# Kernel optimization log

Hardware: AMD Instinct MI355X
Metric: run time of the kernel (lower is better)

## Reference

```python
import jax, jax.numpy as jnp
import numpy as np

H = 2          # h_dim (hard-coded in PPIModel)
L = 4          # n_hid rgcn layers
R = 16         # num_rels
B = 8          # num_bases
N = 1_000_000  # num_nodes
E = 16_000_000 # num_edges


def setup_inputs() -> dict:
    key = jax.random.key(0)
    ks = jax.random.split(key, 10)
    features = jax.random.normal(ks[0], (N * H,), dtype=jnp.float32)
    edge_src = jax.random.randint(ks[1], (E,), 0, N)
    edge_dst = jax.random.randint(ks[2], (E,), 0, N)
    edge_type = jax.random.randint(ks[3], (E,), 0, R)
    norm = jax.random.uniform(ks[4], (E, 1), dtype=jnp.float32)
    # Basis-decomposition params per layer: W_r = sum_b comp[r,b] * V[b]
    V = jax.random.normal(ks[5], (L, B, H, H), dtype=jnp.float32) / np.sqrt(H)
    comp = jax.random.normal(ks[6], (L, R, B), dtype=jnp.float32) / np.sqrt(B)
    bias = jnp.zeros((L, H), dtype=jnp.float32)  # DGL RelGraphConv h_bias (default bias=True)
    w_mlp = jax.random.normal(ks[7], (1, N * H), dtype=jnp.float32) / np.sqrt(N * H)
    b_mlp = jnp.zeros((1,), dtype=jnp.float32)
    return dict(features=features, norm=norm, V=V, comp=comp, bias=bias,
                w_mlp=w_mlp, b_mlp=b_mlp,
                edge_src=edge_src, edge_dst=edge_dst, edge_type=edge_type)


def reference(features, norm, V, comp, bias, w_mlp, b_mlp, edge_src, edge_dst, edge_type):
    x = features.reshape(-1, H)          # [N, 2]
    skip = x
    for i in range(L):
        # relation weights from bases: [R, H, H]
        W = jnp.einsum('rb,bio->rio', comp[i], V[i])
        # message per edge: gather src feats, apply relation weight, scale by norm
        msg = jnp.einsum('ei,eio->eo', x[edge_src], W[edge_type]) * norm  # [E, 2]
        # scatter-sum to destination nodes
        h = jax.ops.segment_sum(msg, edge_dst, num_segments=N) + bias[i]  # [N, 2]
        if i < L - 1:
            h = jax.nn.relu(h)
        x = h
        if i % 2 == 1:
            x = x + skip
            skip = x
    flat = x.reshape(1, N * H)           # [1, 2N]
    logit = flat @ w_mlp.T + b_mlp       # [1, 1]
    return jax.nn.sigmoid(logit)
```

## Files before the change

### kernel.cpp

```cpp
#include <hip/hip_runtime.h>
#include <hip/hip_bf16.h>
#include <hip/hip_fp16.h>

#define HD 2
#define LAYERS 4
#define RELS 16
#define BASES 8

#define NB   512
#define BSH  11
#define SBLK 512
#define TPB  256


__global__ void prep_kernel(const float* __restrict__ V, const float* __restrict__ comp,
                            float* __restrict__ W, float* __restrict__ acc) {
    int idx = threadIdx.x;
    if (idx < LAYERS * RELS * 4) {
        int l  = idx >> 6;
        int r  = (idx >> 2) & (RELS - 1);
        int io = idx & 3;
        float s = 0.f;
        for (int b = 0; b < BASES; ++b)
            s += comp[(l * RELS + r) * BASES + b] * V[(l * BASES + b) * 4 + io];
        W[idx] = s;
    }
    if (idx == 0) *acc = 0.f;
}

__global__ void finalize_kernel(const float* __restrict__ acc,
                                const float* __restrict__ b_mlp,
                                float* __restrict__ out) {
    float v = *acc + b_mlp[0];
    out[0] = 1.f / (1.f + expf(-v));
}


__global__ __launch_bounds__(TPB) void hist_kernel(const int* __restrict__ dst,
                                                   unsigned* __restrict__ blockhist,
                                                   int E, int per) {
    __shared__ unsigned hist[NB];
    for (int i = threadIdx.x; i < NB; i += TPB) hist[i] = 0u;
    __syncthreads();
    int blk = blockIdx.x;
    int e0 = blk * per;
    int e1 = min(e0 + per, E);
    const int4* dst4 = (const int4*)dst;
    int g0 = e0 >> 2, g1 = e1 >> 2;
    for (int g = g0 + threadIdx.x; g < g1; g += TPB) {
        int4 d = dst4[g];
        atomicAdd(&hist[((unsigned)d.x) >> BSH], 1u);
        atomicAdd(&hist[((unsigned)d.y) >> BSH], 1u);
        atomicAdd(&hist[((unsigned)d.z) >> BSH], 1u);
        atomicAdd(&hist[((unsigned)d.w) >> BSH], 1u);
    }
    for (int e = (g1 << 2) + threadIdx.x; e < e1; e += TPB)
        atomicAdd(&hist[((unsigned)dst[e]) >> BSH], 1u);
    __syncthreads();
    for (int i = threadIdx.x; i < NB; i += TPB)
        blockhist[(size_t)blk * NB + i] = hist[i];
}

__global__ __launch_bounds__(TPB) void colscan_kernel(unsigned* __restrict__ blockhist,
                                                      unsigned* __restrict__ totals) {
    int bucket = blockIdx.x;
    int t = threadIdx.x;
    unsigned v0 = blockhist[(size_t)(2 * t)     * NB + bucket];
    unsigned v1 = blockhist[(size_t)(2 * t + 1) * NB + bucket];
    unsigned run = v0 + v1;
    __shared__ unsigned s[TPB];
    s[t] = run;
    __syncthreads();
    for (int off = 1; off < TPB; off <<= 1) {
        unsigned x = (t >= off) ? s[t - off] : 0u;
        __syncthreads();
        s[t] += x;
        __syncthreads();
    }
    unsigned base = s[t] - run;
    blockhist[(size_t)(2 * t)     * NB + bucket] = base;
    blockhist[(size_t)(2 * t + 1) * NB + bucket] = base + v0;
    if (t == TPB - 1) totals[bucket] = s[TPB - 1];
}

__global__ __launch_bounds__(TPB) void scan_kernel(const unsigned* __restrict__ totals,
                                                   unsigned* __restrict__ base) {
    int t = threadIdx.x;
    unsigned v0 = totals[2 * t];
    unsigned v1 = totals[2 * t + 1];
    unsigned run = v0 + v1;
    __shared__ unsigned s[TPB];
    s[t] = run;
    __syncthreads();
    for (int off = 1; off < TPB; off <<= 1) {
        unsigned x = (t >= off) ? s[t - off] : 0u;
        __syncthreads();
        s[t] += x;
        __syncthreads();
    }
    unsigned b0 = s[t] - run;
    base[2 * t]     = b0;
    base[2 * t + 1] = b0 + v0;
    if (t == TPB - 1) base[NB] = s[TPB - 1];
}

__global__ __launch_bounds__(TPB) void scatter_kernel(const int* __restrict__ src,
                                                      const int* __restrict__ dst,
                                                      const int* __restrict__ typ,
                                                      const float* __restrict__ norm,
                                                      const unsigned* __restrict__ blockhist,
                                                      const unsigned* __restrict__ base,
                                                      uint2* __restrict__ packed,
                                                      int E, int per) {
    __shared__ unsigned cnt[NB];
    int blk = blockIdx.x;
    for (int i = threadIdx.x; i < NB; i += TPB)
        cnt[i] = blockhist[(size_t)blk * NB + i] + base[i];
    __syncthreads();
    int e0 = blk * per;
    int e1 = min(e0 + per, E);
    const int4*   src4 = (const int4*)src;
    const int4*   dst4 = (const int4*)dst;
    const int4*   typ4 = (const int4*)typ;
    const float4* nrm4 = (const float4*)norm;
    int g0 = e0 >> 2, g1 = e1 >> 2;

#define PUT(SS, DD, TT, NN)                                                       \
    {                                                                             \
        unsigned _d = (unsigned)(DD);                                             \
        unsigned _bucket = _d >> BSH;                                             \
        unsigned _pos = atomicAdd(&cnt[_bucket], 1u);                             \
        unsigned _w1 = (_d & ((1u << BSH) - 1u)) | (((unsigned)(TT)) << 12) |     \
                       ((unsigned)__half_as_ushort(__float2half_rn(NN)) << 16);   \
        packed[_pos] = make_uint2((unsigned)(SS), _w1);                           \
    }

    for (int g = g0 + threadIdx.x; g < g1; g += TPB) {
        int4 s = src4[g];
        int4 d = dst4[g];
        int4 t = typ4[g];
        float4 nm = nrm4[g];
        PUT(s.x, d.x, t.x, nm.x)
        PUT(s.y, d.y, t.y, nm.y)
        PUT(s.z, d.z, t.z, nm.z)
        PUT(s.w, d.w, t.w, nm.w)
    }
    for (int e = (g1 << 2) + threadIdx.x; e < e1; e += TPB)
        PUT(src[e], dst[e], typ[e], norm[e])
#undef PUT
}

__global__ __launch_bounds__(TPB) void bucket_edge_kernel(
    const uint2* __restrict__ packed,
    const unsigned* __restrict__ base,
    const float2* __restrict__ x2,
    const float* __restrict__ Wl,
    const float* __restrict__ bias2,
    const float2* __restrict__ skip2,
    float2* __restrict__ out2,
    const float2* __restrict__ w2,
    float* __restrict__ acc,
    int N, int do_relu)
{
    __shared__ float acc0[1 << BSH];
    __shared__ float acc1[1 << BSH];
    __shared__ float sW[64];
    __shared__ float wred[4];

    int t = threadIdx.x;
#pragma unroll
    for (int k = 0; k < (1 << BSH) / TPB; ++k) {
        acc0[k * TPB + t] = 0.f;
        acc1[k * TPB + t] = 0.f;
    }
    if (t < 64) sW[t] = Wl[t];
    __syncthreads();

    int b  = blockIdx.x;
    int e0 = (int)base[b];
    int e1 = (int)base[b + 1];

    for (int e = e0 + t; e < e1; e += 2 * TPB) {
        uint2 p0 = packed[e];
        int e2 = e + TPB;
        bool has2 = e2 < e1;
        uint2 p1 = has2 ? packed[e2] : make_uint2(0u, 0u);

        float2 xv0 = x2[p0.x];
        float2 xv1 = has2 ? x2[p1.x] : make_float2(0.f, 0.f);

        {
            unsigned w1  = p0.y;
            unsigned dof = w1 & ((1u << BSH) - 1u);
            int wb = (int)((w1 >> 12) & 15u) << 2;
            float nm = __half2float(__ushort_as_half((unsigned short)(w1 >> 16)));
            float m0 = (xv0.x * sW[wb + 0] + xv0.y * sW[wb + 2]) * nm;
            float m1 = (xv0.x * sW[wb + 1] + xv0.y * sW[wb + 3]) * nm;
            atomicAdd(&acc0[dof], m0);
            atomicAdd(&acc1[dof], m1);
        }
        if (has2) {
            unsigned w1  = p1.y;
            unsigned dof = w1 & ((1u << BSH) - 1u);
            int wb = (int)((w1 >> 12) & 15u) << 2;
            float nm = __half2float(__ushort_as_half((unsigned short)(w1 >> 16)));
            float m0 = (xv1.x * sW[wb + 0] + xv1.y * sW[wb + 2]) * nm;
            float m1 = (xv1.x * sW[wb + 1] + xv1.y * sW[wb + 3]) * nm;
            atomicAdd(&acc0[dof], m0);
            atomicAdd(&acc1[dof], m1);
        }
    }
    __syncthreads();

    float b0 = bias2[0], b1 = bias2[1];
    int nodeBase = b << BSH;
    float part = 0.f;
#pragma unroll
    for (int k = 0; k < (1 << BSH) / TPB; ++k) {
        int i = k * TPB + t;
        int node = nodeBase + i;
        if (node < N) {
            float v0 = acc0[i] + b0;
            float v1 = acc1[i] + b1;
            if (do_relu) { v0 = fmaxf(v0, 0.f); v1 = fmaxf(v1, 0.f); }
            if (skip2) { float2 sv = skip2[node]; v0 += sv.x; v1 += sv.y; }
            if (out2)  out2[node] = make_float2(v0, v1);
            if (w2)    { float2 wv = w2[node]; part += v0 * wv.x + v1 * wv.y; }
        }
    }
    if (w2) {
        for (int off = 32; off > 0; off >>= 1) part += __shfl_down(part, off, 64);
        int lane = t & 63, wv = t >> 6;
        if (lane == 0) wred[wv] = part;
        __syncthreads();
        if (t == 0) atomicAdd(acc, wred[0] + wred[1] + wred[2] + wred[3]);
    }
}


__global__ void zero_kernel(float4* __restrict__ p, int n4) {
    int i = blockIdx.x * blockDim.x + threadIdx.x;
    int stride = gridDim.x * blockDim.x;
    for (; i < n4; i += stride) p[i] = make_float4(0.f, 0.f, 0.f, 0.f);
}

__global__ __launch_bounds__(256) void edge_kernel(
    const float* __restrict__ x, const int* __restrict__ src,
    const int* __restrict__ dst, const int* __restrict__ typ,
    const float* __restrict__ norm, const float* __restrict__ Wl,
    float* __restrict__ h, int E)
{
    __shared__ float sW[64];
    if (threadIdx.x < 64) sW[threadIdx.x] = Wl[threadIdx.x];
    __syncthreads();
    const float2* __restrict__ x2 = (const float2*)x;
    int tid = blockIdx.x * blockDim.x + threadIdx.x;
    int stride = gridDim.x * blockDim.x;
    for (int e = tid; e < E; e += stride) {
        int s = src[e], d = dst[e], t = typ[e];
        float nm = norm[e];
        float2 xv = x2[s];
        int wb = t << 2;
        float m0 = (xv.x * sW[wb + 0] + xv.y * sW[wb + 2]) * nm;
        float m1 = (xv.x * sW[wb + 1] + xv.y * sW[wb + 3]) * nm;
        atomicAdd(&h[2 * (size_t)d],     m0);
        atomicAdd(&h[2 * (size_t)d + 1], m1);
    }
}

__global__ void node_kernel(const float* __restrict__ h, const float* __restrict__ bias_l,
                            const float* __restrict__ skip, float* __restrict__ xout,
                            int N, int do_relu)
{
    float b0 = bias_l[0], b1 = bias_l[1];
    const float2* __restrict__ h2 = (const float2*)h;
    const float2* __restrict__ s2 = (const float2*)skip;
    float2* __restrict__ o2 = (float2*)xout;
    int i = blockIdx.x * blockDim.x + threadIdx.x;
    int stride = gridDim.x * blockDim.x;
    for (; i < N; i += stride) {
        float2 v = h2[i];
        v.x += b0; v.y += b1;
        if (do_relu) { v.x = fmaxf(v.x, 0.f); v.y = fmaxf(v.y, 0.f); }
        if (skip) { float2 sv = s2[i]; v.x += sv.x; v.y += sv.y; }
        o2[i] = v;
    }
}

__global__ __launch_bounds__(256) void dot_kernel(const float* __restrict__ a,
                                                  const float* __restrict__ b,
                                                  float* __restrict__ acc, int n)
{
    int i = blockIdx.x * blockDim.x + threadIdx.x;
    int stride = gridDim.x * blockDim.x;
    float s = 0.f;
    int n4 = n >> 2;
    const float4* __restrict__ a4 = (const float4*)a;
    const float4* __restrict__ b4 = (const float4*)b;
    for (int g = i; g < n4; g += stride) {
        float4 av = a4[g], bv = b4[g];
        s += av.x * bv.x + av.y * bv.y + av.z * bv.z + av.w * bv.w;
    }
    for (int e = (n4 << 2) + i; e < n; e += stride) s += a[e] * b[e];
    for (int off = 32; off > 0; off >>= 1) s += __shfl_down(s, off, 64);
    __shared__ float wsum[4];
    int lane = threadIdx.x & 63, wv = threadIdx.x >> 6;
    if (lane == 0) wsum[wv] = s;
    __syncthreads();
    if (threadIdx.x == 0) atomicAdd(acc, wsum[0] + wsum[1] + wsum[2] + wsum[3]);
}


static inline size_t align256(size_t x) { return (x + 255) & ~(size_t)255; }

extern "C" void kernel_launch(void* const* d_in, const int* in_sizes, int n_in,
                              void* d_out, int out_size, void* d_ws, size_t ws_size,
                              hipStream_t stream) {
    const float* features = (const float*)d_in[0];
    const float* norm     = (const float*)d_in[1];
    const float* V        = (const float*)d_in[2];
    const float* comp     = (const float*)d_in[3];
    const float* bias     = (const float*)d_in[4];
    const float* w_mlp    = (const float*)d_in[5];
    const float* b_mlp    = (const float*)d_in[6];
    const int*   esrc     = (const int*)d_in[7];
    const int*   edst     = (const int*)d_in[8];
    const int*   etyp     = (const int*)d_in[9];

    int NH = in_sizes[0];
    int N  = NH / 2;
    int E  = in_sizes[7];

    char* ws = (char*)d_ws;
    size_t oA    = 0;
    size_t oB    = align256(oA + (size_t)NH * 4);
    size_t oC    = align256(oB + (size_t)NH * 4);
    size_t oW    = align256(oC + (size_t)NH * 4);
    size_t oAcc  = align256(oW + 1024);
    size_t oBase = align256(oAcc + 4);
    size_t oTot  = align256(oBase + (size_t)(NB + 1) * 4);
    size_t oHist = align256(oTot + (size_t)NB * 4);
    size_t oPack = align256(oHist + (size_t)SBLK * NB * 4);
    size_t REQ   = oPack + (size_t)E * 8;

    float* A   = (float*)(ws + oA);
    float* B   = (float*)(ws + oB);
    float* C   = (float*)(ws + oC);
    float* W   = (float*)(ws + oW);
    float* acc = (float*)(ws + oAcc);

    prep_kernel<<<1, 256, 0, stream>>>(V, comp, W, acc);

    if (ws_size >= REQ && N <= (1 << 20)) {
        unsigned* base      = (unsigned*)(ws + oBase);
        unsigned* totals    = (unsigned*)(ws + oTot);
        unsigned* blockhist = (unsigned*)(ws + oHist);
        uint2*    packed    = (uint2*)(ws + oPack);

        int per = (((E + SBLK - 1) / SBLK) + 3) & ~3;

        hist_kernel   <<<SBLK, TPB, 0, stream>>>(edst, blockhist, E, per);
        colscan_kernel<<<NB,   TPB, 0, stream>>>(blockhist, totals);
        scan_kernel   <<<1,    TPB, 0, stream>>>(totals, base);
        scatter_kernel<<<SBLK, TPB, 0, stream>>>(esrc, edst, etyp, norm,
                                                 blockhist, base, packed, E, per);

        int nbkt = (N + (1 << BSH) - 1) >> BSH;
        const float2* feat2 = (const float2*)features;
        const float2* w2    = (const float2*)w_mlp;

        bucket_edge_kernel<<<nbkt, TPB, 0, stream>>>(packed, base, feat2, W + 0,
            bias + 0, nullptr, (float2*)A, nullptr, acc, N, 1);
        bucket_edge_kernel<<<nbkt, TPB, 0, stream>>>(packed, base, (const float2*)A, W + 64,
            bias + 2, feat2, (float2*)B, nullptr, acc, N, 1);
        bucket_edge_kernel<<<nbkt, TPB, 0, stream>>>(packed, base, (const float2*)B, W + 128,
            bias + 4, nullptr, (float2*)C, nullptr, acc, N, 1);
        bucket_edge_kernel<<<nbkt, TPB, 0, stream>>>(packed, base, (const float2*)C, W + 192,
            bias + 6, (const float2*)B, nullptr, w2, acc, N, 0);
    } else {
        int zb = (NH / 4 + 255) / 256;
        int eb = (E / 4 + 255) / 256;
        int nb = (N + 255) / 256;
        int db = (NH / 4 + 255) / 256;

        zero_kernel<<<zb, 256, 0, stream>>>((float4*)A, NH / 4);
        edge_kernel<<<eb, 256, 0, stream>>>(features, esrc, edst, etyp, norm, W + 0, A, E);
        node_kernel<<<nb, 256, 0, stream>>>(A, bias + 0, nullptr, A, N, 1);

        zero_kernel<<<zb, 256, 0, stream>>>((float4*)B, NH / 4);
        edge_kernel<<<eb, 256, 0, stream>>>(A, esrc, edst, etyp, norm, W + 64, B, E);
        node_kernel<<<nb, 256, 0, stream>>>(B, bias + 2, features, B, N, 1);

        zero_kernel<<<zb, 256, 0, stream>>>((float4*)C, NH / 4);
        edge_kernel<<<eb, 256, 0, stream>>>(B, esrc, edst, etyp, norm, W + 128, C, E);
        node_kernel<<<nb, 256, 0, stream>>>(C, bias + 4, nullptr, C, N, 1);

        zero_kernel<<<zb, 256, 0, stream>>>((float4*)A, NH / 4);
        edge_kernel<<<eb, 256, 0, stream>>>(C, esrc, edst, etyp, norm, W + 192, A, E);
        node_kernel<<<nb, 256, 0, stream>>>(A, bias + 6, B, A, N, 0);

        dot_kernel<<<db, 256, 0, stream>>>(A, w_mlp, acc, NH);
    }

    finalize_kernel<<<1, 1, 0, stream>>>(acc, b_mlp, (float*)d_out);
}
```

Before: 1.137 ms.

## Store node features in fp16 and halve scatter block count

Intermediate node activations, and a converted copy of the input features, are now stored as half2 instead of float2. This halves the bytes per random gather in the per-layer edge kernels. Packed edge records are read with nontemporal loads, and the sort's scatter grid is cut from 512 to 256 blocks, with the column scan simplified to match. The cost is reduced precision in the hidden activations and skip connections, plus an extra conversion kernel and workspace.

```diff
diff --git a/kernel.cpp b/kernel.cpp
--- a/kernel.cpp
+++ b/kernel.cpp
@@ -9,7 +9,7 @@
 
 #define NB   512
 #define BSH  11
-#define SBLK 512
+#define SBLK 256
 #define TPB  256
 
 
@@ -35,6 +35,12 @@
     out[0] = 1.f / (1.f + expf(-v));
 }
 
+__global__ __launch_bounds__(TPB) void f2h_kernel(const float2* __restrict__ in,
+                                                  __half2* __restrict__ out, int N) {
+    int i = blockIdx.x * blockDim.x + threadIdx.x;
+    if (i < N) out[i] = __float22half2_rn(in[i]);
+}
+
 
 __global__ __launch_bounds__(TPB) void hist_kernel(const int* __restrict__ dst,
                                                    unsigned* __restrict__ blockhist,
@@ -65,11 +71,9 @@
                                                       unsigned* __restrict__ totals) {
     int bucket = blockIdx.x;
     int t = threadIdx.x;
-    unsigned v0 = blockhist[(size_t)(2 * t)     * NB + bucket];
-    unsigned v1 = blockhist[(size_t)(2 * t + 1) * NB + bucket];
-    unsigned run = v0 + v1;
+    unsigned v = blockhist[(size_t)t * NB + bucket];
     __shared__ unsigned s[TPB];
-    s[t] = run;
+    s[t] = v;
     __syncthreads();
     for (int off = 1; off < TPB; off <<= 1) {
         unsigned x = (t >= off) ? s[t - off] : 0u;
@@ -77,9 +81,7 @@
         s[t] += x;
         __syncthreads();
     }
-    unsigned base = s[t] - run;
-    blockhist[(size_t)(2 * t)     * NB + bucket] = base;
-    blockhist[(size_t)(2 * t + 1) * NB + bucket] = base + v0;
+    blockhist[(size_t)t * NB + bucket] = s[t] - v;
     if (t == TPB - 1) totals[bucket] = s[TPB - 1];
 }
 
@@ -110,7 +112,7 @@
                                                       const float* __restrict__ norm,
                                                       const unsigned* __restrict__ blockhist,
                                                       const unsigned* __restrict__ base,
-                                                      uint2* __restrict__ packed,
+                                                      unsigned long long* __restrict__ packed,
                                                       int E, int per) {
     __shared__ unsigned cnt[NB];
     int blk = blockIdx.x;
@@ -132,7 +134,8 @@
         unsigned _pos = atomicAdd(&cnt[_bucket], 1u);                             \
         unsigned _w1 = (_d & ((1u << BSH) - 1u)) | (((unsigned)(TT)) << 12) |     \
                        ((unsigned)__half_as_ushort(__float2half_rn(NN)) << 16);   \
-        packed[_pos] = make_uint2((unsigned)(SS), _w1);                           \
+        packed[_pos] = (unsigned long long)(unsigned)(SS) |                       \
+                       ((unsigned long long)_w1 << 32);                           \
     }
 
     for (int g = g0 + threadIdx.x; g < g1; g += TPB) {
@@ -151,13 +154,14 @@
 }
 
 __global__ __launch_bounds__(TPB) void bucket_edge_kernel(
-    const uint2* __restrict__ packed,
+    const unsigned long long* __restrict__ packed,
     const unsigned* __restrict__ base,
-    const float2* __restrict__ x2,
+    const __half2* __restrict__ xh,
     const float* __restrict__ Wl,
     const float* __restrict__ bias2,
-    const float2* __restrict__ skip2,
-    float2* __restrict__ out2,
+    const float2* __restrict__ skipF,
+    const __half2* __restrict__ skipH,
+    __half2* __restrict__ outH,
     const float2* __restrict__ w2,
     float* __restrict__ acc,
     int N, int do_relu)
@@ -181,16 +185,16 @@
     int e1 = (int)base[b + 1];
 
     for (int e = e0 + t; e < e1; e += 2 * TPB) {
-        uint2 p0 = packed[e];
+        unsigned long long p0 = __builtin_nontemporal_load(&packed[e]);
         int e2 = e + TPB;
         bool has2 = e2 < e1;
-        uint2 p1 = has2 ? packed[e2] : make_uint2(0u, 0u);
-
-        float2 xv0 = x2[p0.x];
-        float2 xv1 = has2 ? x2[p1.x] : make_float2(0.f, 0.f);
+        unsigned long long p1 = has2 ? __builtin_nontemporal_load(&packed[e2]) : 0ull;
+
+        float2 xv0 = __half22float2(xh[(unsigned)p0]);
+        float2 xv1 = has2 ? __half22float2(xh[(unsigned)p1]) : make_float2(0.f, 0.f);
 
         {
-            unsigned w1  = p0.y;
+            unsigned w1  = (unsigned)(p0 >> 32);
             unsigned dof = w1 & ((1u << BSH) - 1u);
             int wb = (int)((w1 >> 12) & 15u) << 2;
             float nm = __half2float(__ushort_as_half((unsigned short)(w1 >> 16)));
@@ -200,7 +204,7 @@
             atomicAdd(&acc1[dof], m1);
         }
         if (has2) {
-            unsigned w1  = p1.y;
+            unsigned w1  = (unsigned)(p1 >> 32);
             unsigned dof = w1 & ((1u << BSH) - 1u);
             int wb = (int)((w1 >> 12) & 15u) << 2;
             float nm = __half2float(__ushort_as_half((unsigned short)(w1 >> 16)));
@@ -223,8 +227,9 @@
             float v0 = acc0[i] + b0;
             float v1 = acc1[i] + b1;
             if (do_relu) { v0 = fmaxf(v0, 0.f); v1 = fmaxf(v1, 0.f); }
-            if (skip2) { float2 sv = skip2[node]; v0 += sv.x; v1 += sv.y; }
-            if (out2)  out2[node] = make_float2(v0, v1);
+            if (skipF) { float2 sv = skipF[node]; v0 += sv.x; v1 += sv.y; }
+            if (skipH) { float2 sv = __half22float2(skipH[node]); v0 += sv.x; v1 += sv.y; }
+            if (outH)  outH[node] = __floats2half2_rn(v0, v1);
             if (w2)    { float2 wv = w2[node]; part += v0 * wv.x + v1 * wv.y; }
         }
     }
@@ -340,7 +345,11 @@
     size_t oBase = align256(oAcc + 4);
     size_t oTot  = align256(oBase + (size_t)(NB + 1) * 4);
     size_t oHist = align256(oTot + (size_t)NB * 4);
-    size_t oPack = align256(oHist + (size_t)SBLK * NB * 4);
+    size_t oFh   = align256(oHist + (size_t)SBLK * NB * 4);
+    size_t oAh   = align256(oFh + (size_t)N * 4);
+    size_t oBh   = align256(oAh + (size_t)N * 4);
+    size_t oCh   = align256(oBh + (size_t)N * 4);
+    size_t oPack = align256(oCh + (size_t)N * 4);
     size_t REQ   = oPack + (size_t)E * 8;
 
     float* A   = (float*)(ws + oA);
@@ -355,10 +364,15 @@
         unsigned* base      = (unsigned*)(ws + oBase);
         unsigned* totals    = (unsigned*)(ws + oTot);
         unsigned* blockhist = (unsigned*)(ws + oHist);
-        uint2*    packed    = (uint2*)(ws + oPack);
+        __half2*  Fh        = (__half2*)(ws + oFh);
+        __half2*  Ah        = (__half2*)(ws + oAh);
+        __half2*  Bh        = (__half2*)(ws + oBh);
+        __half2*  Ch        = (__half2*)(ws + oCh);
+        unsigned long long* packed = (unsigned long long*)(ws + oPack);
 
         int per = (((E + SBLK - 1) / SBLK) + 3) & ~3;
 
+        f2h_kernel    <<<(N + TPB - 1) / TPB, TPB, 0, stream>>>((const float2*)features, Fh, N);
         hist_kernel   <<<SBLK, TPB, 0, stream>>>(edst, blockhist, E, per);
         colscan_kernel<<<NB,   TPB, 0, stream>>>(blockhist, totals);
         scan_kernel   <<<1,    TPB, 0, stream>>>(totals, base);
@@ -369,14 +383,14 @@
         const float2* feat2 = (const float2*)features;
         const float2* w2    = (const float2*)w_mlp;
 
-        bucket_edge_kernel<<<nbkt, TPB, 0, stream>>>(packed, base, feat2, W + 0,
-            bias + 0, nullptr, (float2*)A, nullptr, acc, N, 1);
-        bucket_edge_kernel<<<nbkt, TPB, 0, stream>>>(packed, base, (const float2*)A, W + 64,
-            bias + 2, feat2, (float2*)B, nullptr, acc, N, 1);
-        bucket_edge_kernel<<<nbkt, TPB, 0, stream>>>(packed, base, (const float2*)B, W + 128,
-            bias + 4, nullptr, (float2*)C, nullptr, acc, N, 1);
-        bucket_edge_kernel<<<nbkt, TPB, 0, stream>>>(packed, base, (const float2*)C, W + 192,
-            bias + 6, (const float2*)B, nullptr, w2, acc, N, 0);
+        bucket_edge_kernel<<<nbkt, TPB, 0, stream>>>(packed, base, Fh, W + 0,
+            bias + 0, nullptr, nullptr, Ah, nullptr, acc, N, 1);
+        bucket_edge_kernel<<<nbkt, TPB, 0, stream>>>(packed, base, Ah, W + 64,
+            bias + 2, feat2, nullptr, Bh, nullptr, acc, N, 1);
+        bucket_edge_kernel<<<nbkt, TPB, 0, stream>>>(packed, base, Bh, W + 128,
+            bias + 4, nullptr, nullptr, Ch, nullptr, acc, N, 1);
+        bucket_edge_kernel<<<nbkt, TPB, 0, stream>>>(packed, base, Ch, W + 192,
+            bias + 6, nullptr, Bh, nullptr, w2, acc, N, 0);
     } else {
         int zb = (NH / 4 + 255) / 256;
         int eb = (E / 4 + 255) / 256;
```

Measured after the change: 1.198 ms. 1.05x slower.
